# Kernel optimization log

Measured on AMD Instinct MI355X. Metric: run time of the kernel, lower is better.

Reference implementation:

```python
import jax, jax.numpy as jnp
import numpy as np

N = 262144
D_IN = 128
ENC_DIMS = [128, 512, 256, 64, 8]   # input -> hidden tanh layers -> linear latent
EST_DIMS = [8, 128, 64, 16]          # latent -> hidden tanh layers -> softmax K
EPS = 1e-6


def setup_inputs() -> dict:
    key = jax.random.key(0)
    ks = jax.random.split(key, 1 + 2 * (len(ENC_DIMS) - 1) + 2 * (len(EST_DIMS) - 1))
    it = iter(ks)
    inp = {"x": jax.random.normal(next(it), (N, D_IN), dtype=jnp.float32)}
    for i in range(len(ENC_DIMS) - 1):
        fan_in, fan_out = ENC_DIMS[i], ENC_DIMS[i + 1]
        inp[f"W{i}"] = jax.random.normal(next(it), (fan_in, fan_out), dtype=jnp.float32) * (1.0 / np.sqrt(fan_in))
        inp[f"b{i}"] = jnp.zeros((fan_out,), dtype=jnp.float32)
    for i in range(len(EST_DIMS) - 1):
        fan_in, fan_out = EST_DIMS[i], EST_DIMS[i + 1]
        inp[f"E{i}"] = jax.random.normal(next(it), (fan_in, fan_out), dtype=jnp.float32) * (1.0 / np.sqrt(fan_in))
        inp[f"eb{i}"] = jnp.zeros((fan_out,), dtype=jnp.float32)
    return inp


def _forward(x, W0, b0, W1, b1, W2, b2, W3, b3, E0, eb0, E1, eb1, E2, eb2):
    # CompressionNet encoder: tanh hidden layers, linear final
    h = jnp.tanh(x @ W0 + b0)
    h = jnp.tanh(h @ W1 + b1)
    h = jnp.tanh(h @ W2 + b2)
    z = h @ W3 + b3                                  # [N, d_z]

    # EstimationNet: tanh hidden layers, softmax final -> gamma [N, K]
    g = jnp.tanh(z @ E0 + eb0)
    g = jnp.tanh(g @ E1 + eb1)
    gamma = jax.nn.softmax(g @ E2 + eb2, axis=1)

    # GMM statistics
    gamma_sum = jnp.sum(gamma, axis=0)               # [K]
    phi = jnp.mean(gamma, axis=0)                    # [K]
    mu = (gamma.T @ z) / gamma_sum[:, None]          # [K, d_z]
    zc_raw = z[:, None, :] - mu[None, :, :]          # [N, K, d_z]
    zc = jnp.sqrt(gamma)[:, :, None] * zc_raw        # [N, K, d_z]
    sigma = jnp.einsum('nkl,nkm->klm', zc, zc) / gamma_sum[:, None, None]  # [K, d, d]
    d_z = z.shape[1]
    L = jnp.linalg.cholesky(sigma + EPS * jnp.eye(d_z, dtype=sigma.dtype)[None])

    # Energy: solve L v = (z - mu)^T per component, [K, d, N]
    v = jax.scipy.linalg.solve_triangular(L, jnp.transpose(zc_raw, (1, 2, 0)), lower=True)
    log_det_sigma = 2.0 * jnp.sum(jnp.log(jnp.diagonal(L, axis1=1, axis2=2)), axis=1)  # [K]
    logits = (jnp.log(phi)[:, None]
              - 0.5 * (jnp.sum(v * v, axis=1)
                       + d_z * jnp.log(2.0 * jnp.pi)
                       + log_det_sigma[:, None]))    # [K, N]
    prob = -jax.scipy.special.logsumexp(logits, axis=0)  # [N]
    return prob, z


def reference(x, W0, b0, W1, b1, W2, b2, W3, b3, E0, eb0, E1, eb1, E2, eb2):
    return _forward(x, W0, b0, W1, b1, W2, b2, W3, b3, E0, eb0, E1, eb1, E2, eb2)
```

## Files before the change

### kernel.cpp

```cpp
#include <hip/hip_runtime.h>
#include <math.h>

#define NSAMP 262144
#define TMS 64

typedef __bf16  bf16x8 __attribute__((ext_vector_type(8)));
typedef __bf16  bf16x4 __attribute__((ext_vector_type(4)));
typedef float   f32x4  __attribute__((ext_vector_type(4)));

__device__ __forceinline__ float fast_tanh(float v) {
  float e = __expf(2.0f * v);
  return 1.0f - 2.0f * __builtin_amdgcn_rcpf(e + 1.0f);
}
__device__ __forceinline__ unsigned short f2bf(float f) {
  unsigned u = __float_as_uint(f);
  unsigned r = (u + 0x7FFFu + ((u >> 16) & 1u)) >> 16;
  return (unsigned short)r;
}

__global__ void k0_pack(const float* __restrict__ W0, const float* __restrict__ W1,
                        const float* __restrict__ W2, const float* __restrict__ E1w,
                        const float* __restrict__ E0w, const float* __restrict__ W3,
                        const float* __restrict__ E2w,
                        unsigned short* __restrict__ wpack)
{
  const int f = blockIdx.x;
  const int lane = threadIdx.x;
  const float* W; int NKS, N, Kreal, Nreal, local;
  if (f < 128)      { W = W0;  NKS = 4;  N = 512; Kreal = 128; Nreal = 512; local = f; }
  else if (f < 384) { W = W1;  NKS = 16; N = 256; Kreal = 512; Nreal = 256; local = f - 128; }
  else if (f < 416) { W = W2;  NKS = 8;  N = 64;  Kreal = 256; Nreal = 64;  local = f - 384; }
  else if (f < 432) { W = E1w; NKS = 4;  N = 64;  Kreal = 128; Nreal = 64;  local = f - 416; }
  else if (f < 440) { W = E0w; NKS = 1;  N = 128; Kreal = 8;   Nreal = 128; local = f - 432; }
  else if (f < 442) { W = W3;  NKS = 2;  N = 8;   Kreal = 64;  Nreal = 8;   local = f - 440; }
  else              { W = E2w; NKS = 2;  N = 16;  Kreal = 64;  Nreal = 16;  local = f - 442; }
  const int nt = local / NKS, ks = local % NKS;
  const int n = nt * 16 + (lane & 15);
  const int kbase = ks * 32 + (lane >> 4) * 8;
  unsigned short* out = wpack + ((size_t)f * 64 + lane) * 8;
#pragma unroll
  for (int i = 0; i < 8; ++i) {
    const int k = kbase + i;
    const float v = (k < Kreal && n < Nreal) ? W[(size_t)k * N + n] : 0.f;
    out[i] = f2bf(v);
  }
}

template<int NTPW>
__device__ __forceinline__ void layer_nks4(
    const char* __restrict__ in, int inRowB, char* __restrict__ outb, int outRowB,
    const unsigned short* __restrict__ wp, int fragBase,
    const float* __restrict__ bias, int lane, int wv)
{
  const int l15 = lane & 15, lg = lane >> 4;
  const int sw = (l15 & 7) << 4;
  bf16x8 a[4][4];
#pragma unroll
  for (int sg = 0; sg < 4; ++sg)
#pragma unroll
    for (int q = 0; q < 4; ++q)
      a[sg][q] = *(const bf16x8*)(in + (sg * 16 + l15) * inRowB + ((q * 64 + lg * 16) ^ sw));
#pragma unroll
  for (int t = 0; t < NTPW; ++t) {
    const int nt = wv * NTPW + t;
    const float4 bv = *(const float4*)(bias + nt * 16 + lg * 4);
    f32x4 acc[4];
#pragma unroll
    for (int sg = 0; sg < 4; ++sg) acc[sg] = {bv.x, bv.y, bv.z, bv.w};
#pragma unroll
    for (int q = 0; q < 4; ++q) {
      const bf16x8 w = *(const bf16x8*)(wp + ((size_t)(fragBase + nt * 4 + q) * 64 + lane) * 8);
#pragma unroll
      for (int sg = 0; sg < 4; ++sg)
        acc[sg] = __builtin_amdgcn_mfma_f32_16x16x32_bf16(w, a[sg][q], acc[sg], 0, 0, 0);
    }
#pragma unroll
    for (int sg = 0; sg < 4; ++sg) {
      bf16x4 tv;
#pragma unroll
      for (int r = 0; r < 4; ++r) tv[r] = (__bf16)fast_tanh(acc[sg][r]);
      *(bf16x4*)(outb + (sg * 16 + l15) * outRowB + ((nt * 32 + lg * 8) ^ sw)) = tv;
    }
  }
}

__device__ __forceinline__ void l2_accum_q(
    const char* __restrict__ H1, const unsigned short* __restrict__ wp,
    int ksOff, f32x4 (&acc)[4][4], int lane, int wv)
{
  const int l15 = lane & 15, lg = lane >> 4;
  const int sw = (l15 & 7) << 4;
  bf16x8 a[4][4];
#pragma unroll
  for (int sg = 0; sg < 4; ++sg)
#pragma unroll
    for (int q = 0; q < 4; ++q)
      a[sg][q] = *(const bf16x8*)(H1 + (sg * 16 + l15) * 256 + ((q * 64 + lg * 16) ^ sw));
#pragma unroll
  for (int t = 0; t < 4; ++t) {
    const int nt = wv * 4 + t;
#pragma unroll
    for (int q = 0; q < 4; ++q) {
      const bf16x8 w = *(const bf16x8*)(wp + ((size_t)(128 + nt * 16 + ksOff + q) * 64 + lane) * 8);
#pragma unroll
      for (int sg = 0; sg < 4; ++sg)
        acc[t][sg] = __builtin_amdgcn_mfma_f32_16x16x32_bf16(w, a[sg][q], acc[t][sg], 0, 0, 0);
    }
  }
}

__device__ __forceinline__ void l3_accum_h(
    const char* __restrict__ H2, const unsigned short* __restrict__ wp,
    int ksOff, f32x4 (&acc)[4], int lane, int wv)
{
  const int l15 = lane & 15, lg = lane >> 4;
  const int sw = (l15 & 7) << 4;
#pragma unroll
  for (int q = 0; q < 4; ++q) {
    const bf16x8 w = *(const bf16x8*)(wp + ((size_t)(384 + wv * 8 + ksOff + q) * 64 + lane) * 8);
#pragma unroll
    for (int sg = 0; sg < 4; ++sg) {
      const bf16x8 a = *(const bf16x8*)(H2 + (sg * 16 + l15) * 256 + ((q * 64 + lg * 16) ^ sw));
      acc[sg] = __builtin_amdgcn_mfma_f32_16x16x32_bf16(w, a, acc[sg], 0, 0, 0);
    }
  }
}

__global__ __launch_bounds__(256, 2) void k1_mfma(
    const float* __restrict__ x, const unsigned short* __restrict__ wpack,
    const float* __restrict__ b0, const float* __restrict__ b1,
    const float* __restrict__ b2, const float* __restrict__ b3,
    const float* __restrict__ eb0, const float* __restrict__ eb1,
    const float* __restrict__ eb2,
    float* __restrict__ zg, float* __restrict__ gamma)
{
  __shared__ char sm[49152];
  char* X   = sm;
  char* H1  = sm + 16384;
  char* H2  = sm + 32768;
  char* L3o = sm;
  char* zb  = sm + 8192;
  char* E0o = sm + 16384;
  char* e1  = sm + 32768;

  const int tid = threadIdx.x;
  const int lane = tid & 63, wv = tid >> 6;
  const int l15 = lane & 15, lg = lane >> 4;
  const int sw = (l15 & 7) << 4;
  const int blk = blockIdx.x;

  {
    const float* xb = x + (size_t)blk * (TMS * 128);
#pragma unroll
    for (int p = 0; p < 8; ++p) {
      const int v = tid + p * 256;
      const float4 t = *(const float4*)(xb + v * 4);
      const int s = v >> 5, k0 = (v & 31) * 4;
      bf16x4 h = {(__bf16)t.x, (__bf16)t.y, (__bf16)t.z, (__bf16)t.w};
      *(bf16x4*)(X + s * 256 + ((k0 * 2) ^ ((s & 7) << 4))) = h;
    }
  }

  f32x4 acc2[4][4];
#pragma unroll
  for (int t = 0; t < 4; ++t) {
    const float4 bv = *(const float4*)(b1 + (wv * 4 + t) * 16 + lg * 4);
#pragma unroll
    for (int sg = 0; sg < 4; ++sg) acc2[t][sg] = {bv.x, bv.y, bv.z, bv.w};
  }
  __syncthreads();

#pragma unroll
  for (int p = 0; p < 4; ++p) {
    layer_nks4<2>(X, 256, H1, 256, wpack, p * 32, b0 + p * 128, lane, wv);
    __syncthreads();
    l2_accum_q(H1, wpack, p * 4, acc2, lane, wv);
    __syncthreads();
  }

  f32x4 acc3[4];
  {
    const float4 bv = *(const float4*)(b2 + wv * 16 + lg * 4);
#pragma unroll
    for (int sg = 0; sg < 4; ++sg) acc3[sg] = {bv.x, bv.y, bv.z, bv.w};
  }

  if (wv < 2) {
#pragma unroll
    for (int t = 0; t < 4; ++t)
#pragma unroll
      for (int sg = 0; sg < 4; ++sg) {
        bf16x4 tv;
#pragma unroll
        for (int r = 0; r < 4; ++r) tv[r] = (__bf16)fast_tanh(acc2[t][sg][r]);
        const int tl = wv * 4 + t;
        *(bf16x4*)(H2 + (sg * 16 + l15) * 256 + ((tl * 32 + lg * 8) ^ sw)) = tv;
      }
  }
  __syncthreads();
  l3_accum_h(H2, wpack, 0, acc3, lane, wv);
  __syncthreads();

  if (wv >= 2) {
#pragma unroll
    for (int t = 0; t < 4; ++t)
#pragma unroll
      for (int sg = 0; sg < 4; ++sg) {
        bf16x4 tv;
#pragma unroll
        for (int r = 0; r < 4; ++r) tv[r] = (__bf16)fast_tanh(acc2[t][sg][r]);
        const int tl = (wv - 2) * 4 + t;
        *(bf16x4*)(H2 + (sg * 16 + l15) * 256 + ((tl * 32 + lg * 8) ^ sw)) = tv;
      }
  }
  __syncthreads();
  l3_accum_h(H2, wpack, 4, acc3, lane, wv);

#pragma unroll
  for (int sg = 0; sg < 4; ++sg) {
    bf16x4 tv;
#pragma unroll
    for (int r = 0; r < 4; ++r) tv[r] = (__bf16)fast_tanh(acc3[sg][r]);
    *(bf16x4*)(L3o + (sg * 16 + l15) * 128 + ((wv * 32 + lg * 8) ^ sw)) = tv;
  }
  __syncthreads();

  {
    bf16x8 a[2];
#pragma unroll
    for (int q = 0; q < 2; ++q)
      a[q] = *(const bf16x8*)(L3o + (wv * 16 + l15) * 128 + ((q * 64 + lg * 16) ^ sw));
    float4 bv = {0.f, 0.f, 0.f, 0.f};
    if (lg < 2) bv = *(const float4*)(b3 + lg * 4);
    f32x4 acc = {bv.x, bv.y, bv.z, bv.w};
#pragma unroll
    for (int q = 0; q < 2; ++q) {
      const bf16x8 w = *(const bf16x8*)(wpack + ((size_t)(440 + q) * 64 + lane) * 8);
      acc = __builtin_amdgcn_mfma_f32_16x16x32_bf16(w, a[q], acc, 0, 0, 0);
    }
    if (lg < 2) {
      *(f32x4*)(zg + ((size_t)blk * 64 + wv * 16 + l15) * 8 + lg * 4) = acc;
      bf16x4 zv;
#pragma unroll
      for (int r = 0; r < 4; ++r) zv[r] = (__bf16)acc[r];
      *(bf16x4*)(zb + (wv * 16 + l15) * 16 + lg * 8) = zv;
    }
  }
  __syncthreads();

  {
    bf16x8 az[4];
#pragma unroll
    for (int sg = 0; sg < 4; ++sg)
      az[sg] = *(const bf16x8*)(zb + (sg * 16 + l15) * 16);
#pragma unroll
    for (int t = 0; t < 2; ++t) {
      const int nt = wv * 2 + t;
      const float4 bv = *(const float4*)(eb0 + nt * 16 + lg * 4);
      const bf16x8 w = *(const bf16x8*)(wpack + ((size_t)(432 + nt) * 64 + lane) * 8);
#pragma unroll
      for (int sg = 0; sg < 4; ++sg) {
        f32x4 acc = {bv.x, bv.y, bv.z, bv.w};
        acc = __builtin_amdgcn_mfma_f32_16x16x32_bf16(w, az[sg], acc, 0, 0, 0);
        bf16x4 tv;
#pragma unroll
        for (int r = 0; r < 4; ++r) tv[r] = (__bf16)fast_tanh(acc[r]);
        *(bf16x4*)(E0o + (sg * 16 + l15) * 256 + ((nt * 32 + lg * 8) ^ sw)) = tv;
      }
    }
  }
  __syncthreads();

  layer_nks4<1>(E0o, 256, e1, 128, wpack, 416, eb1, lane, wv);
  __syncthreads();

  {
    bf16x8 a[2];
#pragma unroll
    for (int q = 0; q < 2; ++q)
      a[q] = *(const bf16x8*)(e1 + (wv * 16 + l15) * 128 + ((q * 64 + lg * 16) ^ sw));
    const float4 bv = *(const float4*)(eb2 + lg * 4);
    f32x4 acc = {bv.x, bv.y, bv.z, bv.w};
#pragma unroll
    for (int q = 0; q < 2; ++q) {
      const bf16x8 w = *(const bf16x8*)(wpack + ((size_t)(442 + q) * 64 + lane) * 8);
      acc = __builtin_amdgcn_mfma_f32_16x16x32_bf16(w, a[q], acc, 0, 0, 0);
    }
    float m = fmaxf(fmaxf(acc[0], acc[1]), fmaxf(acc[2], acc[3]));
    m = fmaxf(m, __shfl_xor(m, 16));
    m = fmaxf(m, __shfl_xor(m, 32));
    float e0v = __expf(acc[0] - m), e1v = __expf(acc[1] - m);
    float e2v = __expf(acc[2] - m), e3v = __expf(acc[3] - m);
    float s = e0v + e1v + e2v + e3v;
    s += __shfl_xor(s, 16);
    s += __shfl_xor(s, 32);
    const float inv = __builtin_amdgcn_rcpf(s);
    float4 g = {e0v * inv, e1v * inv, e2v * inv, e3v * inv};
    *(float4*)(gamma + ((size_t)blk * 64 + wv * 16 + l15) * 16 + lg * 4) = g;
  }
}

__global__ __launch_bounds__(256) void k2a_partial(
    const float* __restrict__ zg, const float* __restrict__ gamma,
    float* __restrict__ part)
{
  __shared__ float zl[256 * 8];
  __shared__ float gl[256 * 16];
  __shared__ float red[4][16][46];
  const int tid = threadIdx.x;
  const int blk = blockIdx.x;
  const int s0 = blk * 256;

  {
    const float4 a = *(const float4*)(zg + (size_t)(s0 + tid) * 8);
    const float4 b = *(const float4*)(zg + (size_t)(s0 + tid) * 8 + 4);
    *(float4*)(&zl[tid * 8])     = a;
    *(float4*)(&zl[tid * 8 + 4]) = b;
  }
  {
    const float* gp = gamma + (size_t)(s0 + tid) * 16;
#pragma unroll
    for (int q = 0; q < 4; ++q)
      *(float4*)(&gl[tid * 16 + q * 4]) = *(const float4*)(gp + q * 4);
  }
  __syncthreads();

  const int k = tid & 15, sub = tid >> 4;
  float m2[36], m1[8], gs = 0.f;
#pragma unroll
  for (int i = 0; i < 36; ++i) m2[i] = 0.f;
#pragma unroll
  for (int i = 0; i < 8; ++i) m1[i] = 0.f;

#pragma unroll 4
  for (int i = 0; i < 16; ++i) {
    const int n = i * 16 + sub;
    const float4 za = *(const float4*)(&zl[n * 8]);
    const float4 zb4 = *(const float4*)(&zl[n * 8 + 4]);
    const float zv[8] = {za.x, za.y, za.z, za.w, zb4.x, zb4.y, zb4.z, zb4.w};
    const float g = gl[n * 16 + k];
    gs += g;
    float t[8];
#pragma unroll
    for (int l = 0; l < 8; ++l) { t[l] = g * zv[l]; m1[l] += t[l]; }
    int p = 0;
#pragma unroll
    for (int l = 0; l < 8; ++l)
#pragma unroll
      for (int m = l; m < 8; ++m) {
        m2[p] = fmaf(t[l], zv[m], m2[p]);
        ++p;
      }
  }

#pragma unroll
  for (int i = 0; i < 36; ++i) {
    m2[i] += __shfl_xor(m2[i], 16);
    m2[i] += __shfl_xor(m2[i], 32);
  }
#pragma unroll
  for (int i = 0; i < 8; ++i) {
    m1[i] += __shfl_xor(m1[i], 16);
    m1[i] += __shfl_xor(m1[i], 32);
  }
  gs += __shfl_xor(gs, 16);
  gs += __shfl_xor(gs, 32);

  const int lane = tid & 63, wv = tid >> 6;
  if (lane < 16) {
#pragma unroll
    for (int i = 0; i < 36; ++i) red[wv][lane][i] = m2[i];
#pragma unroll
    for (int i = 0; i < 8; ++i) red[wv][lane][36 + i] = m1[i];
    red[wv][lane][44] = gs;
  }
  __syncthreads();

  for (int o = tid; o < 768; o += 256) {
    const int kk = o / 48, p = o % 48;
    float v = 0.f;
    if (p < 45)
      v = red[0][kk][p] + red[1][kk][p] + red[2][kk][p] + red[3][kk][p];
    part[(size_t)blk * 768 + o] = v;
  }
}

__global__ __launch_bounds__(256) void k2b_reduce(
    const float* __restrict__ part, float* __restrict__ stats)
{
  const int oi = blockIdx.x % 3, jc = blockIdx.x / 3;
  const int o = oi * 256 + threadIdx.x;
  float s = 0.f;
#pragma unroll 4
  for (int j = jc * 128; j < jc * 128 + 128; ++j)
    s += part[(size_t)j * 768 + o];
  atomicAdd(&stats[o], s);
}

__global__ void k3_finalize(const float* __restrict__ stats, float* __restrict__ coef)
{
  const int k = threadIdx.x;
  if (k >= 16) return;
  const float* sk = stats + k * 48;
  const float gs = sk[44];
  float mu[8];
#pragma unroll
  for (int l = 0; l < 8; ++l) mu[l] = sk[36 + l] / gs;

  float S[8][8];
  {
    int p = 0;
    for (int l = 0; l < 8; ++l)
      for (int m = l; m < 8; ++m) {
        const float v = sk[p++] / gs - mu[l] * mu[m];
        S[l][m] = v; S[m][l] = v;
      }
  }
  for (int l = 0; l < 8; ++l) S[l][l] += 1e-6f;

  float L[8][8];
  for (int i = 0; i < 8; ++i)
    for (int j = 0; j <= i; ++j) {
      float s = S[i][j];
      for (int t = 0; t < j; ++t) s -= L[i][t] * L[j][t];
      if (i == j) L[i][i] = sqrtf(s);
      else        L[i][j] = s / L[j][j];
    }
  float logdet = 0.f;
  for (int i = 0; i < 8; ++i) logdet += logf(L[i][i]);
  logdet *= 2.f;

  float U[8][8];
  for (int j = 0; j < 8; ++j) {
    U[j][j] = 1.f / L[j][j];
    for (int i = j + 1; i < 8; ++i) {
      float s = 0.f;
      for (int t = j; t < i; ++t) s += L[i][t] * U[t][j];
      U[i][j] = -s / L[i][i];
    }
  }
  float Amat[8][8];
  for (int l = 0; l < 8; ++l)
    for (int m = l; m < 8; ++m) {
      float s = 0.f;
      for (int i = m; i < 8; ++i) s += U[i][l] * U[i][m];
      Amat[l][m] = s; Amat[m][l] = s;
    }
  float c[8];
  for (int l = 0; l < 8; ++l) {
    float s = 0.f;
    for (int m = 0; m < 8; ++m) s += Amat[l][m] * mu[m];
    c[l] = s;
  }
  float muAmu = 0.f;
  for (int l = 0; l < 8; ++l) muAmu += c[l] * mu[l];

  const float LOG2PI = 1.8378770664093453f;
  const float cnst = logf(gs) - logf((float)NSAMP)
                   - 0.5f * (8.f * LOG2PI + logdet + muAmu);

  float* ck = coef + k * 48;
  {
    int p = 0;
    for (int l = 0; l < 8; ++l)
      for (int m = l; m < 8; ++m) {
        ck[p] = (l == m) ? (-0.5f * Amat[l][l]) : (-Amat[l][m]);
        ++p;
      }
  }
  for (int l = 0; l < 8; ++l) ck[36 + l] = c[l];
  ck[44] = cnst;
  ck[45] = 0.f; ck[46] = 0.f; ck[47] = 0.f;
}

__global__ __launch_bounds__(256) void k4_energy(
    const float* __restrict__ zg, const float* __restrict__ coef,
    float* __restrict__ prob)
{
  __shared__ float C[16 * 48];
  for (int i = threadIdx.x; i < 16 * 48; i += 256) C[i] = coef[i];
  __syncthreads();

  const int n = blockIdx.x * 256 + threadIdx.x;
  const float4 za = *(const float4*)(zg + (size_t)n * 8);
  const float4 zb = *(const float4*)(zg + (size_t)n * 8 + 4);
  const float z[8] = {za.x, za.y, za.z, za.w, zb.x, zb.y, zb.z, zb.w};

  float pr[36];
  {
    int p = 0;
#pragma unroll
    for (int l = 0; l < 8; ++l)
#pragma unroll
      for (int m = l; m < 8; ++m) pr[p++] = z[l] * z[m];
  }

  float mx = -1e30f, sm = 0.f;
#pragma unroll
  for (int k = 0; k < 16; ++k) {
    const float4* c4 = (const float4*)&C[k * 48];
    float acc = C[k * 48 + 44];
#pragma unroll
    for (int q = 0; q < 9; ++q) {
      const float4 t = c4[q];
      acc = fmaf(t.x, pr[q * 4 + 0], acc);
      acc = fmaf(t.y, pr[q * 4 + 1], acc);
      acc = fmaf(t.z, pr[q * 4 + 2], acc);
      acc = fmaf(t.w, pr[q * 4 + 3], acc);
    }
    {
      const float4 t = c4[9];
      acc = fmaf(t.x, z[0], acc); acc = fmaf(t.y, z[1], acc);
      acc = fmaf(t.z, z[2], acc); acc = fmaf(t.w, z[3], acc);
    }
    {
      const float4 t = c4[10];
      acc = fmaf(t.x, z[4], acc); acc = fmaf(t.y, z[5], acc);
      acc = fmaf(t.z, z[6], acc); acc = fmaf(t.w, z[7], acc);
    }
    const float nm = fmaxf(mx, acc);
    sm = sm * __expf(mx - nm) + __expf(acc - nm);
    mx = nm;
  }
  prob[n] = -(mx + __logf(sm));
}

extern "C" void kernel_launch(void* const* d_in, const int* in_sizes, int n_in,
                              void* d_out, int out_size, void* d_ws, size_t ws_size,
                              hipStream_t stream)
{
  const float* x   = (const float*)d_in[0];
  const float* W0  = (const float*)d_in[1];
  const float* b0  = (const float*)d_in[2];
  const float* W1  = (const float*)d_in[3];
  const float* b1  = (const float*)d_in[4];
  const float* W2  = (const float*)d_in[5];
  const float* b2  = (const float*)d_in[6];
  const float* W3  = (const float*)d_in[7];
  const float* b3  = (const float*)d_in[8];
  const float* E0w = (const float*)d_in[9];
  const float* eb0 = (const float*)d_in[10];
  const float* E1w = (const float*)d_in[11];
  const float* eb1 = (const float*)d_in[12];
  const float* E2w = (const float*)d_in[13];
  const float* eb2 = (const float*)d_in[14];

  float* out  = (float*)d_out;
  float* prob = out;
  float* zg   = out + NSAMP;

  unsigned short* wpack = (unsigned short*)d_ws;
  float* ws    = (float*)d_ws;
  float* gamma = ws + 114688;
  float* stats = gamma + (size_t)NSAMP * 16;
  float* coef  = stats + 768;
  float* part  = coef + 768;

  hipMemsetAsync(stats, 0, 768 * sizeof(float), stream);

  k0_pack<<<444, 64, 0, stream>>>(W0, W1, W2, E1w, E0w, W3, E2w, wpack);
  k1_mfma<<<NSAMP / TMS, 256, 0, stream>>>(x, wpack, b0, b1, b2, b3,
                                           eb0, eb1, eb2, zg, gamma);
  k2a_partial<<<1024, 256, 0, stream>>>(zg, gamma, part);
  k2b_reduce<<<24, 256, 0, stream>>>(part, stats);
  k3_finalize<<<1, 64, 0, stream>>>(stats, coef);
  k4_energy<<<NSAMP / 256, 256, 0, stream>>>(zg, coef, prob);
}
```

Baseline: 218.3 us.

## Halve fused MLP tile to 32 samples and compute layer 3 in one pass

Shrinks the per-block sample tile of the fused encoder/estimator kernel from 64 to 32 rows. This halves accumulator registers and shared memory, which should allow more resident blocks and more latency hiding. Because H2 now fits at full width, layer 3 runs as a single K=256 pass instead of two half passes with extra barriers. In exchange, each block gets half as much weight reuse per fragment load, and wave 2-3 sit idle in the final z and softmax stages.

```diff
diff --git a/kernel.cpp b/kernel.cpp
--- a/kernel.cpp
+++ b/kernel.cpp
@@ -2,7 +2,7 @@
 #include <math.h>
 
 #define NSAMP 262144
-#define TMS 64
+#define TMS 32
 
 typedef __bf16  bf16x8 __attribute__((ext_vector_type(8)));
 typedef __bf16  bf16x4 __attribute__((ext_vector_type(4)));
@@ -54,9 +54,9 @@
 {
   const int l15 = lane & 15, lg = lane >> 4;
   const int sw = (l15 & 7) << 4;
-  bf16x8 a[4][4];
-#pragma unroll
-  for (int sg = 0; sg < 4; ++sg)
+  bf16x8 a[2][4];
+#pragma unroll
+  for (int sg = 0; sg < 2; ++sg)
 #pragma unroll
     for (int q = 0; q < 4; ++q)
       a[sg][q] = *(const bf16x8*)(in + (sg * 16 + l15) * inRowB + ((q * 64 + lg * 16) ^ sw));
@@ -64,18 +64,18 @@
   for (int t = 0; t < NTPW; ++t) {
     const int nt = wv * NTPW + t;
     const float4 bv = *(const float4*)(bias + nt * 16 + lg * 4);
-    f32x4 acc[4];
-#pragma unroll
-    for (int sg = 0; sg < 4; ++sg) acc[sg] = {bv.x, bv.y, bv.z, bv.w};
+    f32x4 acc[2];
+#pragma unroll
+    for (int sg = 0; sg < 2; ++sg) acc[sg] = {bv.x, bv.y, bv.z, bv.w};
 #pragma unroll
     for (int q = 0; q < 4; ++q) {
       const bf16x8 w = *(const bf16x8*)(wp + ((size_t)(fragBase + nt * 4 + q) * 64 + lane) * 8);
 #pragma unroll
-      for (int sg = 0; sg < 4; ++sg)
+      for (int sg = 0; sg < 2; ++sg)
         acc[sg] = __builtin_amdgcn_mfma_f32_16x16x32_bf16(w, a[sg][q], acc[sg], 0, 0, 0);
     }
 #pragma unroll
-    for (int sg = 0; sg < 4; ++sg) {
+    for (int sg = 0; sg < 2; ++sg) {
       bf16x4 tv;
 #pragma unroll
       for (int r = 0; r < 4; ++r) tv[r] = (__bf16)fast_tanh(acc[sg][r]);
@@ -86,13 +86,13 @@
 
 __device__ __forceinline__ void l2_accum_q(
     const char* __restrict__ H1, const unsigned short* __restrict__ wp,
-    int ksOff, f32x4 (&acc)[4][4], int lane, int wv)
+    int ksOff, f32x4 (&acc)[4][2], int lane, int wv)
 {
   const int l15 = lane & 15, lg = lane >> 4;
   const int sw = (l15 & 7) << 4;
-  bf16x8 a[4][4];
-#pragma unroll
-  for (int sg = 0; sg < 4; ++sg)
+  bf16x8 a[2][4];
+#pragma unroll
+  for (int sg = 0; sg < 2; ++sg)
 #pragma unroll
     for (int q = 0; q < 4; ++q)
       a[sg][q] = *(const bf16x8*)(H1 + (sg * 16 + l15) * 256 + ((q * 64 + lg * 16) ^ sw));
@@ -103,25 +103,8 @@
     for (int q = 0; q < 4; ++q) {
       const bf16x8 w = *(const bf16x8*)(wp + ((size_t)(128 + nt * 16 + ksOff + q) * 64 + lane) * 8);
 #pragma unroll
-      for (int sg = 0; sg < 4; ++sg)
+      for (int sg = 0; sg < 2; ++sg)
         acc[t][sg] = __builtin_amdgcn_mfma_f32_16x16x32_bf16(w, a[sg][q], acc[t][sg], 0, 0, 0);
-    }
-  }
-}
-
-__device__ __forceinline__ void l3_accum_h(
-    const char* __restrict__ H2, const unsigned short* __restrict__ wp,
-    int ksOff, f32x4 (&acc)[4], int lane, int wv)
-{
-  const int l15 = lane & 15, lg = lane >> 4;
-  const int sw = (l15 & 7) << 4;
-#pragma unroll
-  for (int q = 0; q < 4; ++q) {
-    const bf16x8 w = *(const bf16x8*)(wp + ((size_t)(384 + wv * 8 + ksOff + q) * 64 + lane) * 8);
-#pragma unroll
-    for (int sg = 0; sg < 4; ++sg) {
-      const bf16x8 a = *(const bf16x8*)(H2 + (sg * 16 + l15) * 256 + ((q * 64 + lg * 16) ^ sw));
-      acc[sg] = __builtin_amdgcn_mfma_f32_16x16x32_bf16(w, a, acc[sg], 0, 0, 0);
     }
   }
 }
@@ -134,14 +117,14 @@
     const float* __restrict__ eb2,
     float* __restrict__ zg, float* __restrict__ gamma)
 {
-  __shared__ char sm[49152];
+  __shared__ char sm[32768];
   char* X   = sm;
-  char* H1  = sm + 16384;
-  char* H2  = sm + 32768;
+  char* H1  = sm + 8192;
+  char* H2  = sm + 16384;
   char* L3o = sm;
-  char* zb  = sm + 8192;
-  char* E0o = sm + 16384;
-  char* e1  = sm + 32768;
+  char* zb  = sm + 4096;
+  char* E0o = sm + 8192;
+  char* e1  = sm + 16384;
 
   const int tid = threadIdx.x;
   const int lane = tid & 63, wv = tid >> 6;
@@ -152,7 +135,7 @@
   {
     const float* xb = x + (size_t)blk * (TMS * 128);
 #pragma unroll
-    for (int p = 0; p < 8; ++p) {
+    for (int p = 0; p < 4; ++p) {
       const int v = tid + p * 256;
       const float4 t = *(const float4*)(xb + v * 4);
       const int s = v >> 5, k0 = (v & 31) * 4;
@@ -161,12 +144,12 @@
     }
   }
 
-  f32x4 acc2[4][4];
+  f32x4 acc2[4][2];
 #pragma unroll
   for (int t = 0; t < 4; ++t) {
     const float4 bv = *(const float4*)(b1 + (wv * 4 + t) * 16 + lg * 4);
 #pragma unroll
-    for (int sg = 0; sg < 4; ++sg) acc2[t][sg] = {bv.x, bv.y, bv.z, bv.w};
+    for (int sg = 0; sg < 2; ++sg) acc2[t][sg] = {bv.x, bv.y, bv.z, bv.w};
   }
   __syncthreads();
 
@@ -178,54 +161,42 @@
     __syncthreads();
   }
 
-  f32x4 acc3[4];
-  {
+#pragma unroll
+  for (int t = 0; t < 4; ++t)
+#pragma unroll
+    for (int sg = 0; sg < 2; ++sg) {
+      bf16x4 tv;
+#pragma unroll
+      for (int r = 0; r < 4; ++r) tv[r] = (__bf16)fast_tanh(acc2[t][sg][r]);
+      *(bf16x4*)(H2 + (sg * 16 + l15) * 512 + (((wv * 4 + t) * 32 + lg * 8) ^ sw)) = tv;
+    }
+  __syncthreads();
+
+  {
+    f32x4 acc3[2];
     const float4 bv = *(const float4*)(b2 + wv * 16 + lg * 4);
 #pragma unroll
-    for (int sg = 0; sg < 4; ++sg) acc3[sg] = {bv.x, bv.y, bv.z, bv.w};
-  }
+    for (int sg = 0; sg < 2; ++sg) acc3[sg] = {bv.x, bv.y, bv.z, bv.w};
+#pragma unroll
+    for (int q = 0; q < 8; ++q) {
+      const bf16x8 w = *(const bf16x8*)(wpack + ((size_t)(384 + wv * 8 + q) * 64 + lane) * 8);
+#pragma unroll
+      for (int sg = 0; sg < 2; ++sg) {
+        const bf16x8 a = *(const bf16x8*)(H2 + (sg * 16 + l15) * 512 + ((q * 64 + lg * 16) ^ sw));
+        acc3[sg] = __builtin_amdgcn_mfma_f32_16x16x32_bf16(w, a, acc3[sg], 0, 0, 0);
+      }
+    }
+#pragma unroll
+    for (int sg = 0; sg < 2; ++sg) {
+      bf16x4 tv;
+#pragma unroll
+      for (int r = 0; r < 4; ++r) tv[r] = (__bf16)fast_tanh(acc3[sg][r]);
+      *(bf16x4*)(L3o + (sg * 16 + l15) * 128 + ((wv * 32 + lg * 8) ^ sw)) = tv;
+    }
+  }
+  __syncthreads();
 
   if (wv < 2) {
-#pragma unroll
-    for (int t = 0; t < 4; ++t)
-#pragma unroll
-      for (int sg = 0; sg < 4; ++sg) {
-        bf16x4 tv;
-#pragma unroll
-        for (int r = 0; r < 4; ++r) tv[r] = (__bf16)fast_tanh(acc2[t][sg][r]);
-        const int tl = wv * 4 + t;
-        *(bf16x4*)(H2 + (sg * 16 + l15) * 256 + ((tl * 32 + lg * 8) ^ sw)) = tv;
-      }
-  }
-  __syncthreads();
-  l3_accum_h(H2, wpack, 0, acc3, lane, wv);
-  __syncthreads();
-
-  if (wv >= 2) {
-#pragma unroll
-    for (int t = 0; t < 4; ++t)
-#pragma unroll
-      for (int sg = 0; sg < 4; ++sg) {
-        bf16x4 tv;
-#pragma unroll
-        for (int r = 0; r < 4; ++r) tv[r] = (__bf16)fast_tanh(acc2[t][sg][r]);
-        const int tl = (wv - 2) * 4 + t;
-        *(bf16x4*)(H2 + (sg * 16 + l15) * 256 + ((tl * 32 + lg * 8) ^ sw)) = tv;
-      }
-  }
-  __syncthreads();
-  l3_accum_h(H2, wpack, 4, acc3, lane, wv);
-
-#pragma unroll
-  for (int sg = 0; sg < 4; ++sg) {
-    bf16x4 tv;
-#pragma unroll
-    for (int r = 0; r < 4; ++r) tv[r] = (__bf16)fast_tanh(acc3[sg][r]);
-    *(bf16x4*)(L3o + (sg * 16 + l15) * 128 + ((wv * 32 + lg * 8) ^ sw)) = tv;
-  }
-  __syncthreads();
-
-  {
     bf16x8 a[2];
 #pragma unroll
     for (int q = 0; q < 2; ++q)
@@ -239,7 +210,7 @@
       acc = __builtin_amdgcn_mfma_f32_16x16x32_bf16(w, a[q], acc, 0, 0, 0);
     }
     if (lg < 2) {
-      *(f32x4*)(zg + ((size_t)blk * 64 + wv * 16 + l15) * 8 + lg * 4) = acc;
+      *(f32x4*)(zg + ((size_t)blk * 32 + wv * 16 + l15) * 8 + lg * 4) = acc;
       bf16x4 zv;
 #pragma unroll
       for (int r = 0; r < 4; ++r) zv[r] = (__bf16)acc[r];
@@ -249,9 +220,9 @@
   __syncthreads();
 
   {
-    bf16x8 az[4];
-#pragma unroll
-    for (int sg = 0; sg < 4; ++sg)
+    bf16x8 az[2];
+#pragma unroll
+    for (int sg = 0; sg < 2; ++sg)
       az[sg] = *(const bf16x8*)(zb + (sg * 16 + l15) * 16);
 #pragma unroll
     for (int t = 0; t < 2; ++t) {
@@ -259,7 +230,7 @@
       const float4 bv = *(const float4*)(eb0 + nt * 16 + lg * 4);
       const bf16x8 w = *(const bf16x8*)(wpack + ((size_t)(432 + nt) * 64 + lane) * 8);
 #pragma unroll
-      for (int sg = 0; sg < 4; ++sg) {
+      for (int sg = 0; sg < 2; ++sg) {
         f32x4 acc = {bv.x, bv.y, bv.z, bv.w};
         acc = __builtin_amdgcn_mfma_f32_16x16x32_bf16(w, az[sg], acc, 0, 0, 0);
         bf16x4 tv;
@@ -274,7 +245,7 @@
   layer_nks4<1>(E0o, 256, e1, 128, wpack, 416, eb1, lane, wv);
   __syncthreads();
 
-  {
+  if (wv < 2) {
     bf16x8 a[2];
 #pragma unroll
     for (int q = 0; q < 2; ++q)
@@ -296,7 +267,7 @@
     s += __shfl_xor(s, 32);
     const float inv = __builtin_amdgcn_rcpf(s);
     float4 g = {e0v * inv, e1v * inv, e2v * inv, e3v * inv};
-    *(float4*)(gamma + ((size_t)blk * 64 + wv * 16 + l15) * 16 + lg * 4) = g;
+    *(float4*)(gamma + ((size_t)blk * 32 + wv * 16 + l15) * 16 + lg * 4) = g;
   }
 }
 
```

Result: slower. 236.2 us (+8.2%).
